# Kernel optimization log

Measured on AMD Instinct MI355X. Metric: run time of the kernel, lower is better.

The kernel has to match this reference:

```python
import jax, jax.numpy as jnp
import numpy as np
import math

# ----- sizes -----
NUM_EDGES = 16384
NUM_NODES = 1024          # senders index into [0, NUM_NODES)
N_MUL = 64                # multiplicity n = V.shape[1]
AVG_NEIGH = 16.0          # avg_num_neighbors
F_IN = 64                 # scalar feature dim of x

# ----- real spherical harmonics (component normalization: sum_m Y_lm^2 = 2l+1) -----
_S3 = math.sqrt(3.0); _S5 = math.sqrt(5.0); _S15 = math.sqrt(15.0)
_C33 = math.sqrt(70.0)/4.0; _C32 = math.sqrt(105.0)/2.0
_C31 = math.sqrt(42.0)/4.0; _C30 = math.sqrt(7.0)/2.0; _CXYZ = math.sqrt(105.0)

def _sph(vn):
    x, y, z = vn[:, 0], vn[:, 1], vn[:, 2]
    Y0 = jnp.ones_like(x)[:, None]
    Y1 = _S3 * vn
    Y2 = jnp.stack([_S15*x*y, _S15*y*z, 0.5*_S5*(3*z*z - 1), _S15*x*z, 0.5*_S15*(x*x - y*y)], axis=1)
    Y3 = jnp.stack([_C33*y*(3*x*x - y*y), _CXYZ*x*y*z, _C31*y*(5*z*z - 1), _C30*z*(5*z*z - 3), _C31*x*(5*z*z - 1), _C32*z*(x*x - y*y), _C33*x*(x*x - 3*y*y)], axis=1)
    return [Y0, Y1, Y2, Y3]

# monomial form of the same SH, used to derive EXACT Clebsch-Gordan coefficients
_SHP = {
    0: [[(1.0, (0,0,0))]],
    1: [[(_S3, (1,0,0))], [(_S3, (0,1,0))], [(_S3, (0,0,1))]],
    2: [[(_S15, (1,1,0))], [(_S15, (0,1,1))], [(1.5*_S5, (0,0,2)), (-0.5*_S5, (0,0,0))], [(_S15, (1,0,1))], [(0.5*_S15, (2,0,0)), (-0.5*_S15, (0,2,0))]],
    3: [[(3*_C33, (2,1,0)), (-_C33, (0,3,0))], [(_CXYZ, (1,1,1))], [(5*_C31, (0,1,2)), (-_C31, (0,1,0))], [(5*_C30, (0,0,3)), (-3*_C30, (0,0,1))], [(5*_C31, (1,0,2)), (-_C31, (1,0,0))], [(_C32, (2,0,1)), (-_C32, (0,2,1))], [(_C33, (3,0,0)), (-3*_C33, (1,2,0))]],
}

def _dfact(n):
    r = 1
    while n > 1:
        r *= n; n -= 2
    return r

def _mono_int(e):
    # exact integral of x^a y^b z^c over the unit sphere
    a, b, c = e
    if (a % 2) or (b % 2) or (c % 2):
        return 0.0
    return 4.0*math.pi*_dfact(a-1)*_dfact(b-1)*_dfact(c-1)/_dfact(a+b+c+1)

def _pmul(p, q):
    return [(cp*cq, (a1+a2, b1+b2, c1+c2)) for cp, (a1,b1,c1) in p for cq, (a2,b2,c2) in q]

def _pint(p):
    return sum(c*_mono_int(e) for c, e in p)

def _cg(l1, l2, l3):
    # unique SO(3) intertwiner in this real-SH basis, scaled like e3nn component norm: sqrt(2l3+1)*w3j
    C = np.zeros((2*l1+1, 2*l2+1, 2*l3+1))
    for i, p1 in enumerate(_SHP[l1]):
        for j, p2 in enumerate(_SHP[l2]):
            p12 = _pmul(p1, p2)
            for k, p3 in enumerate(_SHP[l3]):
                C[i, j, k] = _pint(_pmul(p12, p3)) / (4.0*math.pi)
    return jnp.asarray(C / np.linalg.norm(C) * np.sqrt(2*l3+1), dtype=jnp.float32)

# tensor-product paths surviving filter_ir_out = 0e + 1o + 2e (inputs: SH 0e+1o+2e+3o, V 0e+1o+2e)
_PATHS0 = [(0,0), (1,1), (2,2)]
_PATHS1 = [(0,1), (1,0), (1,2), (2,1), (3,2)]
_PATHS2 = [(0,2), (1,1), (2,0), (2,2), (3,1)]
CGS = {(l1, l2, l3): _cg(l1, l2, l3) for l3, ps in ((0, _PATHS0), (1, _PATHS1), (2, _PATHS2)) for l1, l2 in ps}

# e3nn normalize_function(silu): divide by sqrt(E_{z~N(0,1)}[silu(z)^2])
_zg = np.linspace(-12.0, 12.0, 200001)
_phi = np.exp(-0.5*_zg*_zg)/np.sqrt(2.0*np.pi)
_sl = _zg/(1.0 + np.exp(-_zg))
ACT_C = float(np.sqrt(np.sum(_sl*_sl*_phi)*(_zg[1]-_zg[0])))

def _nsilu(v):
    return jax.nn.silu(v) / ACT_C

def _forward(vectors, x, V, senders, W_w, W1, W2, W3, Wv1, Wv2):
    E, n = V.shape[0], V.shape[1]
    d = jnp.linalg.norm(vectors, axis=1, keepdims=True)                 # [E,1] edge lengths
    vn = vectors / d
    Y = jnp.concatenate(_sph(vn), axis=1)                               # [E,16], ell = 0..3
    w = (x @ W_w) / math.sqrt(x.shape[1])                               # [E,n] edge weights (1-layer MLP, no act)
    wY = w[:, :, None] * Y[:, None, :]                                  # [E,n,16]
    agg = jax.ops.segment_sum(wY, senders, num_segments=NUM_NODES)[senders]  # scatter_sum + map_back
    agg = agg / math.sqrt(AVG_NEIGH)
    A = jnp.split(agg, [1, 4, 9], axis=2)                               # SH chunks: dims 1,3,5,7
    B = jnp.split(V, [1, 4], axis=2)                                    # V chunks: dims 1,3,5
    def tp(l1, l2, l3):
        return jnp.einsum('eni,enj,ijk->enk', A[l1], B[l2], CGS[(l1, l2, l3)])
    scal = jnp.concatenate([tp(a, b, 0) for a, b in _PATHS0], axis=2)   # [E,n,3] new scalars
    V1 = jnp.concatenate([tp(a, b, 1) for a, b in _PATHS1], axis=1)     # [E,5n,3] 1o paths
    V2 = jnp.concatenate([tp(a, b, 2) for a, b in _PATHS2], axis=1)     # [E,5n,5] 2e paths
    h = jnp.concatenate([x, scal.reshape(E, 3*n)], axis=1)              # [E, F_IN+3n]
    h = _nsilu(h @ W1 / math.sqrt(h.shape[1]))
    h = _nsilu(h @ W2 / math.sqrt(W2.shape[0]))
    h = h @ W3 / math.sqrt(W3.shape[0])                                 # output_activation=False
    # poly_envelope(p-1=5, 2), p=6: 1 - 28 d^6 + 48 d^7 - 21 d^8 on [0,1), 0 outside
    u = 1.0 - 28.0*d**6 + 48.0*d**7 - 21.0*d**8
    x_out = jnp.where(d < 1.0, u, 0.0) * h                              # [E,64]
    o1 = jnp.einsum('emi,mo->eoi', V1, Wv1) / math.sqrt(V1.shape[1])    # Linear per irrep: [E,n,3]
    o2 = jnp.einsum('emi,mo->eoi', V2, Wv2) / math.sqrt(V2.shape[1])    # [E,n,5]
    # output 0e block has no input path -> zeros (e3nn Linear, no bias)
    V_out = jnp.concatenate([jnp.zeros((E, n, 1), x_out.dtype), o1, o2], axis=2)  # [E,n,9]
    return x_out, V_out

def setup_inputs():
    key = jax.random.key(0)
    ks = jax.random.split(key, 10)
    E = NUM_EDGES
    vectors = 0.35 * jax.random.normal(ks[0], (E, 3), jnp.float32)   # mostly inside cutoff radius 1
    x = jax.random.normal(ks[1], (E, F_IN), jnp.float32)
    V = jax.random.normal(ks[2], (E, N_MUL, 9), jnp.float32)
    senders = jax.random.randint(ks[3], (E,), 0, NUM_NODES, dtype=jnp.int32)
    W_w = jax.random.normal(ks[4], (F_IN, N_MUL), jnp.float32)
    W1 = jax.random.normal(ks[5], (F_IN + 3*N_MUL, 64), jnp.float32)
    W2 = jax.random.normal(ks[6], (64, 64), jnp.float32)
    W3 = jax.random.normal(ks[7], (64, 64), jnp.float32)
    Wv1 = jax.random.normal(ks[8], (5*N_MUL, N_MUL), jnp.float32)
    Wv2 = jax.random.normal(ks[9], (5*N_MUL, N_MUL), jnp.float32)
    return {"vectors": vectors, "x": x, "V": V, "senders": senders, "W_w": W_w, "W1": W1, "W2": W2, "W3": W3, "Wv1": Wv1, "Wv2": Wv2}

def reference(vectors, x, V, senders, W_w, W1, W2, W3, Wv1, Wv2):
    return _forward(vectors, x, V, senders, W_w, W1, W2, W3, Wv1, Wv2)
```

## Files before the change

### kernel.cpp

```cpp
#include <hip/hip_runtime.h>
#include <math.h>

#define NNODES 1024
#define EB 4

typedef __attribute__((ext_vector_type(8))) short short8;
typedef __attribute__((ext_vector_type(4))) float f32x4;

__device__ __forceinline__ unsigned short f2bf(float f) {
  union { float f; unsigned int u; } v; v.f = f;
  unsigned int r = v.u + 0x7fffu + ((v.u >> 16) & 1u);
  return (unsigned short)(r >> 16);
}

struct CGPack { float v[576]; };

static const double H_SHC[16][2] = {
  {1.0, 0.0},
  {1.7320508075688772, 0.0},
  {1.7320508075688772, 0.0},
  {1.7320508075688772, 0.0},
  {3.8729833462074170, 0.0},
  {3.8729833462074170, 0.0},
  {3.3541019662496844, -1.1180339887498949},
  {3.8729833462074170, 0.0},
  {1.9364916731037085, -1.9364916731037085},
  {6.2749501990055667, -2.0916500663351889},
  {10.246950765959598, 0.0},
  {8.1009258730098255, -1.6201851746019651},
  {6.6143782776614768, -3.9686269665968861},
  {8.1009258730098255, -1.6201851746019651},
  {5.1234753829797990, -5.1234753829797990},
  {2.0916500663351889, -6.2749501990055667},
};
static const int H_SHE[16][2] = {
  {0,0},{1,0},{16,0},{256,0},
  {17,0},{272,0},{512,0},{257,0},{2,32},
  {18,48},{273,0},{528,16},{768,256},{513,1},{258,288},{3,33}};
static const int H_PL1[13] = {0,1,2, 0,1,1,2,3, 0,1,2,2,3};
static const int H_PL2[13] = {0,1,2, 1,0,2,1,2, 2,1,0,2,1};
static const int H_PL3[13] = {0,0,0, 1,1,1,1,1, 2,2,2,2,2};
static const int H_PCG[13] = {0,1,10, 35,44,53,98,143, 248,273,318,343,468};

static double h_dfact(int n) { double r = 1.0; while (n > 1) { r *= n; n -= 2; } return r; }

struct HostConsts {
  CGPack pack;
  float inv_actc;
  HostConsts() {
    const int LOFF[4] = {0,1,4,9};
    for (int p = 0; p < 13; p++) {
      int l1 = H_PL1[p], l2 = H_PL2[p], l3 = H_PL3[p];
      int n1 = 2*l1+1, n2 = 2*l2+1, n3 = 2*l3+1, nent = n1*n2*n3;
      double vals[125], ss = 0.0;
      for (int t = 0; t < nent; t++) {
        int i = t / (n2*n3);
        int rem = t - i*(n2*n3);
        int j = rem / n3;
        int k = rem - j*n3;
        int lm1 = LOFF[l1]+i, lm2 = LOFF[l2]+j, lm3 = LOFF[l3]+k;
        double v = 0.0;
        for (int t1 = 0; t1 < 2; t1++)
        for (int t2 = 0; t2 < 2; t2++)
        for (int t3 = 0; t3 < 2; t3++) {
          double cc = H_SHC[lm1][t1]*H_SHC[lm2][t2]*H_SHC[lm3][t3];
          if (cc == 0.0) continue;
          int s = H_SHE[lm1][t1] + H_SHE[lm2][t2] + H_SHE[lm3][t3];
          int a = s & 15, b = (s >> 4) & 15, c = (s >> 8) & 15;
          if (!((a|b|c) & 1))
            v += cc * (h_dfact(a-1)*h_dfact(b-1)*h_dfact(c-1) / h_dfact(a+b+c+1));
        }
        vals[t] = v; ss += v*v;
      }
      double scale = sqrt((double)(2*l3+1)) / sqrt(ss);
      for (int t = 0; t < nent; t++) pack.v[H_PCG[p]+t] = (float)(vals[t]*scale*0.25);
    }
    pack.v[573] = pack.v[574] = pack.v[575] = 0.f;
    double s = 0.0, dz = 24.0/200000.0;
    for (int i = 0; i <= 200000; i++) {
      double z = -12.0 + dz*i;
      double ph = exp(-0.5*z*z) * 0.39894228040143267794;
      double sl = z / (1.0 + exp(-z));
      s += sl*sl*ph;
    }
    inv_actc = (float)(1.0 / sqrt(s*dz));
  }
};

__global__ __launch_bounds__(256) void k_pre(
    const int* __restrict__ senders, int* __restrict__ counts, int* __restrict__ elist,
    const float* __restrict__ x, const float* __restrict__ Ww,
    float* __restrict__ w_ws,
    const float* __restrict__ Wv1, const float* __restrict__ Wv2,
    const float* __restrict__ W1, const float* __restrict__ W2, const float* __restrict__ W3,
    unsigned short* __restrict__ wv1f, unsigned short* __restrict__ wv2f,
    unsigned short* __restrict__ w1f, unsigned short* __restrict__ w2f,
    unsigned short* __restrict__ w3f,
    float inv_actc, int E)
{
  const int t = threadIdx.x;
  const int bid = blockIdx.x;
  const int nsc = (E + 255) >> 8;

  if (bid < nsc) {
    int e = bid*256 + t;
    if (e < E) {
      int s = senders[e];
      int pos = atomicAdd(&counts[s], 1) & 63;
      elist[s*64 + pos] = e;
    }
    return;
  }

  if (bid < nsc + 32) {
    const int wid = t >> 6, lane = t & 63;
    const int g = (bid - nsc)*4 + wid;
    const float ia = inv_actc;
    const float s320 = 0.05590169943749474f;
    const float* src; unsigned short* dst; int nk, f; float sc;
    if (g < 40)       { src = Wv1; dst = wv1f; nk = 10; f = g;       sc = s320; }
    else if (g < 80)  { src = Wv2; dst = wv2f; nk = 10; f = g - 40;  sc = s320; }
    else if (g < 112) { src = W1;  dst = w1f;  nk = 8;  f = g - 80;  sc = 0.0625f; }
    else if (g < 120) { src = W2;  dst = w2f;  nk = 2;  f = g - 112; sc = 0.125f*ia; }
    else              { src = W3;  dst = w3f;  nk = 2;  f = g - 120; sc = 0.125f*ia; }
    int nt = f / nk;
    int ks = f - nt*nk;
    unsigned short us[8];
    #pragma unroll
    for (int j = 0; j < 8; j++) {
      float v = src[(ks*32 + (lane>>4)*8 + j)*64 + nt*16 + (lane & 15)];
      us[j] = f2bf(v * sc);
    }
    uint4 pk;
    pk.x = (unsigned)us[0] | ((unsigned)us[1] << 16);
    pk.y = (unsigned)us[2] | ((unsigned)us[3] << 16);
    pk.z = (unsigned)us[4] | ((unsigned)us[5] << 16);
    pk.w = (unsigned)us[6] | ((unsigned)us[7] << 16);
    *(uint4*)(dst + ((size_t)f*64 + lane)*8) = pk;
    return;
  }

  __shared__ float xsh[64*64];
  const int eb0 = (bid - nsc - 32) * 64;
  for (int q = t; q < 1024; q += 256)
    ((f32x4*)xsh)[q] = ((const f32x4*)(x + (size_t)eb0*64))[q];

  const int n = t & 63;
  float ww[64];
  #pragma unroll
  for (int f = 0; f < 64; f++) ww[f] = Ww[f*64 + n];
  __syncthreads();

  const int er0 = (t >> 6) * 16;
  #pragma unroll
  for (int i = 0; i < 16; i++) {
    int e = er0 + i;
    const f32x4* xr = (const f32x4*)(&xsh[e*64]);
    float a0 = 0.f, a1 = 0.f, a2 = 0.f, a3 = 0.f;
    #pragma unroll
    for (int fq = 0; fq < 16; fq += 4) {
      f32x4 x0 = xr[fq+0], x1 = xr[fq+1], x2 = xr[fq+2], x3 = xr[fq+3];
      a0 = fmaf(x0.x, ww[fq*4+0],  fmaf(x0.y, ww[fq*4+1],  fmaf(x0.z, ww[fq*4+2],  fmaf(x0.w, ww[fq*4+3],  a0))));
      a1 = fmaf(x1.x, ww[fq*4+4],  fmaf(x1.y, ww[fq*4+5],  fmaf(x1.z, ww[fq*4+6],  fmaf(x1.w, ww[fq*4+7],  a1))));
      a2 = fmaf(x2.x, ww[fq*4+8],  fmaf(x2.y, ww[fq*4+9],  fmaf(x2.z, ww[fq*4+10], fmaf(x2.w, ww[fq*4+11], a2))));
      a3 = fmaf(x3.x, ww[fq*4+12], fmaf(x3.y, ww[fq*4+13], fmaf(x3.z, ww[fq*4+14], fmaf(x3.w, ww[fq*4+15], a3))));
    }
    w_ws[(size_t)(eb0+e)*64 + n] = ((a0+a1)+(a2+a3)) * 0.125f;
  }
}

__global__ __launch_bounds__(256) void k_node(
    const float* __restrict__ vec, const float* __restrict__ w_ws,
    const int* __restrict__ counts, const int* __restrict__ elist,
    float* __restrict__ node_agg)
{
  __shared__ float red[4*1024];
  const int wid = threadIdx.x >> 6, lane = threadIdx.x & 63;
  const int s = blockIdx.x;
  const int deg = min(counts[s], 64);

  const float S3 = 1.7320508075688772f, S5 = 2.23606797749979f, S15 = 3.872983346207417f;
  const float C33 = 2.091650066335189f, C32 = 5.123475382979799f, C31 = 1.6201851746019651f;
  const float C30 = 1.3228756555322954f, CX = 10.246950765959598f;

  float A[16];
  #pragma unroll
  for (int k = 0; k < 16; k++) A[k] = 0.f;

  for (int ii = wid; ii < deg; ii += 4) {
    int e = elist[s*64 + ii];
    float wv = w_ws[(size_t)e*64 + lane];
    float vx = vec[e*3+0], vy = vec[e*3+1], vz = vec[e*3+2];
    float d = sqrtf(vx*vx + vy*vy + vz*vz);
    float X = vx/d, Yv = vy/d, Z = vz/d;
    float y[16];
    y[0] = 1.f;
    y[1] = S3*X;  y[2] = S3*Yv;  y[3] = S3*Z;
    y[4] = S15*X*Yv; y[5] = S15*Yv*Z; y[6] = 0.5f*S5*(3.f*Z*Z - 1.f);
    y[7] = S15*X*Z;  y[8] = 0.5f*S15*(X*X - Yv*Yv);
    y[9]  = C33*Yv*(3.f*X*X - Yv*Yv);
    y[10] = CX*X*Yv*Z;
    y[11] = C31*Yv*(5.f*Z*Z - 1.f);
    y[12] = C30*Z*(5.f*Z*Z - 3.f);
    y[13] = C31*X*(5.f*Z*Z - 1.f);
    y[14] = C32*Z*(X*X - 3.f*Yv*Yv)*0.f + C32*Z*(X*X - Yv*Yv);
    y[14] = C32*Z*(X*X - Yv*Yv);
    y[15] = C33*X*(X*X - 3.f*Yv*Yv);
    #pragma unroll
    for (int k = 0; k < 16; k++) A[k] = fmaf(wv, y[k], A[k]);
  }
  #pragma unroll
  for (int k = 0; k < 16; k++) red[wid*1024 + lane*16 + k] = A[k];
  __syncthreads();
  const int t = threadIdx.x;
  f32x4 v0 = ((f32x4*)red)[t];
  f32x4 v1 = ((f32x4*)red)[256 + t];
  f32x4 v2 = ((f32x4*)red)[512 + t];
  f32x4 v3 = ((f32x4*)red)[768 + t];
  f32x4 sum = v0 + v1 + v2 + v3;
  ((f32x4*)(node_agg + (size_t)s*1024))[t] = sum;
}

template<int L1, int L2, int L3>
__device__ __forceinline__ void tp_path(const float* __restrict__ cgp,
    const float a[16], const float b[9], float o[2*L3+1])
{
  constexpr int N1 = 2*L1+1, N2 = 2*L2+1, N3 = 2*L3+1;
  constexpr int AO = (L1==0) ? 0 : (L1==1) ? 1 : (L1==2) ? 4 : 9;
  constexpr int BO = (L2==0) ? 0 : (L2==1) ? 1 : 4;
  constexpr int LM1 = (L1==0) ? 0 : (L1==1) ? 1 : (L1==2) ? 4 : 9;
  constexpr int LM2 = (L2==0) ? 0 : (L2==1) ? 1 : 4;
  constexpr int LM3 = (L3==0) ? 0 : (L3==1) ? 1 : 4;
  static constexpr unsigned char PAR[16] =
      {0, 1,2,4, 3,6,0,5,0, 2,7,2,4,1,4,1};
  #pragma unroll
  for (int k = 0; k < N3; k++) o[k] = 0.f;
  int ci = 0;
  #pragma unroll
  for (int i = 0; i < N1; i++) {
    #pragma unroll
    for (int j = 0; j < N2; j++) {
      float ab = a[AO+i] * b[BO+j];
      #pragma unroll
      for (int k = 0; k < N3; k++) {
        if ((PAR[LM1+i] ^ PAR[LM2+j] ^ PAR[LM3+k]) == 0)
          o[k] = fmaf(ab, cgp[ci], o[k]);
        ci++;
      }
    }
  }
}

__global__ __launch_bounds__(256, 6) void edge_main(
    const float* __restrict__ vec, const float* __restrict__ x,
    const float* __restrict__ V, const int* __restrict__ senders,
    const float* __restrict__ node_agg, const CGPack P,
    const unsigned short* __restrict__ wv1f, const unsigned short* __restrict__ wv2f,
    const unsigned short* __restrict__ w1f, const unsigned short* __restrict__ w2f,
    const unsigned short* __restrict__ w3f,
    float* __restrict__ out, int E)
{
  __shared__ __align__(16) unsigned short V12sh[32*328];
  __shared__ __align__(16) unsigned short zrow[336];
  __shared__ __align__(16) unsigned short hsh[4*264];
  __shared__ __align__(16) unsigned short h1sh[4*72];
  __shared__ __align__(16) unsigned short h2sh[4*72];
  __shared__ __align__(16) float xosh[4*64];
  __shared__ float ush[EB];

  unsigned short* V1sh = V12sh;
  unsigned short* V2sh = V12sh + 12*328;
  float* vosh = (float*)V12sh;

  const float* cg = P.v;

  const int t = threadIdx.x;
  const int wid = t >> 6, lane = t & 63;
  const int e0 = blockIdx.x * EB;
  const size_t E64 = (size_t)E * 64;

  if (t < 168) ((unsigned int*)zrow)[t] = 0u;

  if (t < 64) {
    int el = t >> 4, off = (t & 15)*4;
    f32x4 xv = *(const f32x4*)(x + (size_t)(e0 + el)*64 + off);
    uint2 pk;
    pk.x = (unsigned)f2bf(xv.x) | ((unsigned)f2bf(xv.y) << 16);
    pk.y = (unsigned)f2bf(xv.z) | ((unsigned)f2bf(xv.w) << 16);
    *(uint2*)(hsh + el*264 + off) = pk;
  }

  {
    const int eloc = wid;
    const int eg = e0 + eloc;

    float b[9];
    const float* vp = V + (size_t)eg*576 + lane*9;
    #pragma unroll
    for (int j = 0; j < 9; j++) b[j] = vp[j];

    const int s = senders[eg];
    float a[16];
    const f32x4* nap = (const f32x4*)(node_agg + s*1024 + lane*16);
    #pragma unroll
    for (int q = 0; q < 4; q++) {
      f32x4 av = nap[q];
      a[q*4+0] = av.x; a[q*4+1] = av.y; a[q*4+2] = av.z; a[q*4+3] = av.w;
    }

    float o1[1], o3[3], o5[5];
    tp_path<0,0,0>(cg + 0,  a, b, o1); hsh[eloc*264 + 64 + lane*3 + 0] = f2bf(o1[0]);
    tp_path<1,1,0>(cg + 1,  a, b, o1); hsh[eloc*264 + 64 + lane*3 + 1] = f2bf(o1[0]);
    tp_path<2,2,0>(cg + 10, a, b, o1); hsh[eloc*264 + 64 + lane*3 + 2] = f2bf(o1[0]);
    tp_path<0,1,1>(cg + 35, a, b, o3);
    { int r = eloc*3; for (int i=0;i<3;i++) V1sh[(r+i)*328 + 0*64 + lane] = f2bf(o3[i]); }
    tp_path<1,0,1>(cg + 44, a, b, o3);
    { int r = eloc*3; for (int i=0;i<3;i++) V1sh[(r+i)*328 + 1*64 + lane] = f2bf(o3[i]); }
    tp_path<1,2,1>(cg + 53, a, b, o3);
    { int r = eloc*3; for (int i=0;i<3;i++) V1sh[(r+i)*328 + 2*64 + lane] = f2bf(o3[i]); }
    tp_path<2,1,1>(cg + 98, a, b, o3);
    { int r = eloc*3; for (int i=0;i<3;i++) V1sh[(r+i)*328 + 3*64 + lane] = f2bf(o3[i]); }
    tp_path<3,2,1>(cg + 143, a, b, o3);
    { int r = eloc*3; for (int i=0;i<3;i++) V1sh[(r+i)*328 + 4*64 + lane] = f2bf(o3[i]); }
    tp_path<0,2,2>(cg + 248, a, b, o5);
    { int r = eloc*5; for (int i=0;i<5;i++) V2sh[(r+i)*328 + 0*64 + lane] = f2bf(o5[i]); }
    tp_path<1,1,2>(cg + 273, a, b, o5);
    { int r = eloc*5; for (int i=0;i<5;i++) V2sh[(r+i)*328 + 1*64 + lane] = f2bf(o5[i]); }
    tp_path<2,0,2>(cg + 318, a, b, o5);
    { int r = eloc*5; for (int i=0;i<5;i++) V2sh[(r+i)*328 + 2*64 + lane] = f2bf(o5[i]); }
    tp_path<2,2,2>(cg + 343, a, b, o5);
    { int r = eloc*5; for (int i=0;i<5;i++) V2sh[(r+i)*328 + 3*64 + lane] = f2bf(o5[i]); }
    tp_path<3,1,2>(cg + 468, a, b, o5);
    { int r = eloc*5; for (int i=0;i<5;i++) V2sh[(r+i)*328 + 4*64 + lane] = f2bf(o5[i]); }

    if (lane == 0) {
      float vx = vec[eg*3+0], vy = vec[eg*3+1], vz = vec[eg*3+2];
      float d = sqrtf(vx*vx + vy*vy + vz*vz);
      float u = 0.f;
      if (d < 1.f) {
        float d3 = d*d*d, d6 = d3*d3, d7 = d6*d, d8 = d7*d;
        u = 1.f - 28.f*d6 + 48.f*d7 - 21.f*d8;
      }
      ush[eloc] = u;
    }
  }
  __syncthreads();

  const int ntile = wid;
  const int qr = lane >> 4;
  const int ml = lane & 15;

  f32x4 acc1 = (f32x4){0,0,0,0};
  {
    const unsigned short* p0 = (ml < 12) ? &V1sh[ml*328] : zrow;
    const unsigned short* bb = wv1f + ((size_t)(ntile*10)*64 + lane)*8;
    #pragma unroll
    for (int ks = 0; ks < 10; ks++) {
      short8 bf = *(const short8*)(bb + ks*512);
      short8 af = *(const short8*)(p0 + ks*32 + qr*8);
      acc1 = __builtin_amdgcn_mfma_f32_16x16x32_bf16(af, bf, acc1, 0, 0, 0);
    }
  }

  f32x4 acc2a = (f32x4){0,0,0,0}, acc2b = (f32x4){0,0,0,0};
  {
    const unsigned short* p0 = &V2sh[ml*328];
    const unsigned short* p1 = (16+ml < 20) ? &V2sh[(16+ml)*328] : zrow;
    const unsigned short* bb = wv2f + ((size_t)(ntile*10)*64 + lane)*8;
    #pragma unroll
    for (int ks = 0; ks < 10; ks++) {
      short8 bf = *(const short8*)(bb + ks*512);
      int ao = ks*32 + qr*8;
      short8 af0 = *(const short8*)(p0 + ao);
      short8 af1 = *(const short8*)(p1 + ao);
      acc2a = __builtin_amdgcn_mfma_f32_16x16x32_bf16(af0, bf, acc2a, 0, 0, 0);
      acc2b = __builtin_amdgcn_mfma_f32_16x16x32_bf16(af1, bf, acc2b, 0, 0, 0);
    }
  }

  const unsigned short* hp = (ml < 4) ? &hsh[ml*264] : zrow;
  {
    f32x4 c = (f32x4){0,0,0,0};
    const unsigned short* bb = w1f + ((size_t)(ntile*8)*64 + lane)*8;
    #pragma unroll
    for (int ks = 0; ks < 8; ks++) {
      short8 bf = *(const short8*)(bb + ks*512);
      short8 af = *(const short8*)(hp + ks*32 + qr*8);
      c = __builtin_amdgcn_mfma_f32_16x16x32_bf16(af, bf, c, 0, 0, 0);
    }
    #pragma unroll
    for (int r = 0; r < 4; r++) {
      int row = qr*4 + r;
      if (row < 4) {
        float v = c[r];
        float sv = v / (1.f + expf(-v));
        h1sh[row*72 + ntile*16 + ml] = f2bf(sv);
      }
    }
  }
  __syncthreads();

  #pragma unroll
  for (int r = 0; r < 4; r++) {
    int row = qr*4 + r;
    if (row < 12) {
      int el = row / 3, i = row - (row/3)*3;
      vosh[el*584 + (ntile*16+ml)*9 + 1 + i] = acc1[r];
    }
  }
  #pragma unroll
  for (int r = 0; r < 4; r++) {
    int row = qr*4 + r;
    int el = row / 5, i = row - (row/5)*5;
    vosh[el*584 + (ntile*16+ml)*9 + 4 + i] = acc2a[r];
  }
  #pragma unroll
  for (int r = 0; r < 4; r++) {
    int row = 16 + qr*4 + r;
    if (row < 20) {
      int el = row / 5, i = row - (row/5)*5;
      vosh[el*584 + (ntile*16+ml)*9 + 4 + i] = acc2b[r];
    }
  }
  { int el = t >> 6, o = t & 63;
    vosh[el*584 + o*9] = 0.f; }

  {
    f32x4 c = (f32x4){0,0,0,0};
    const unsigned short* ap = (ml < 4) ? &h1sh[ml*72] : zrow;
    const unsigned short* bb = w2f + ((size_t)(ntile*2)*64 + lane)*8;
    #pragma unroll
    for (int ks = 0; ks < 2; ks++) {
      short8 bf = *(const short8*)(bb + ks*512);
      short8 af = *(const short8*)(ap + ks*32 + qr*8);
      c = __builtin_amdgcn_mfma_f32_16x16x32_bf16(af, bf, c, 0, 0, 0);
    }
    #pragma unroll
    for (int r = 0; r < 4; r++) {
      int row = qr*4 + r;
      if (row < 4) {
        float v = c[r];
        float sv = v / (1.f + expf(-v));
        h2sh[row*72 + ntile*16 + ml] = f2bf(sv);
      }
    }
  }
  __syncthreads();

  {
    f32x4 c = (f32x4){0,0,0,0};
    const unsigned short* ap = (ml < 4) ? &h2sh[ml*72] : zrow;
    const unsigned short* bb = w3f + ((size_t)(ntile*2)*64 + lane)*8;
    #pragma unroll
    for (int ks = 0; ks < 2; ks++) {
      short8 bf = *(const short8*)(bb + ks*512);
      short8 af = *(const short8*)(ap + ks*32 + qr*8);
      c = __builtin_amdgcn_mfma_f32_16x16x32_bf16(af, bf, c, 0, 0, 0);
    }
    #pragma unroll
    for (int r = 0; r < 4; r++) {
      int row = qr*4 + r;
      if (row < 4) xosh[row*64 + ntile*16 + ml] = ush[row] * c[r];
    }
  }

  for (int q = t; q < 576; q += 256) {
    int el = q / 144, i4 = q - (q/144)*144;
    ((f32x4*)(out + E64 + (size_t)(e0+el)*576))[i4] = ((f32x4*)(vosh + el*584))[i4];
  }
  __syncthreads();

  if (t < 64)
    ((f32x4*)(out + (size_t)e0*64))[t] = ((f32x4*)xosh)[t];
}

extern "C" void kernel_launch(void* const* d_in, const int* in_sizes, int n_in,
                              void* d_out, int out_size, void* d_ws, size_t ws_size,
                              hipStream_t stream)
{
  const float* vec     = (const float*)d_in[0];
  const float* x       = (const float*)d_in[1];
  const float* V       = (const float*)d_in[2];
  const int*   senders = (const int*)  d_in[3];
  const float* Ww      = (const float*)d_in[4];
  const float* W1      = (const float*)d_in[5];
  const float* W2      = (const float*)d_in[6];
  const float* W3      = (const float*)d_in[7];
  const float* Wv1     = (const float*)d_in[8];
  const float* Wv2     = (const float*)d_in[9];
  float* out = (float*)d_out;
  const int E = in_sizes[0] / 3;

  static HostConsts HC;

  char* base = (char*)d_ws;
  float* node_agg = (float*)(base);
  float* w_ws     = (float*)(base + (4<<20));
  int* counts     = (int*)  (base + (8<<20) + 8192);
  int* elist      = (int*)  (base + (8<<20) + 12288);
  unsigned short* wv1f = (unsigned short*)(base + (8<<20) + 278528);
  unsigned short* wv2f = (unsigned short*)(base + (8<<20) + 319488);
  unsigned short* w1f  = (unsigned short*)(base + (8<<20) + 360448);
  unsigned short* w2f  = (unsigned short*)(base + (8<<20) + 393216);
  unsigned short* w3f  = (unsigned short*)(base + (8<<20) + 401408);

  hipMemsetAsync(counts, 0, NNODES*sizeof(int), stream);

  const int nsc = (E + 255) >> 8;
  const int ngemm = (E + 63) >> 6;
  k_pre<<<nsc + 32 + ngemm, 256, 0, stream>>>(senders, counts, elist,
                                      x, Ww, w_ws,
                                      Wv1, Wv2, W1, W2, W3,
                                      wv1f, wv2f, w1f, w2f, w3f, HC.inv_actc, E);
  k_node<<<NNODES, 256, 0, stream>>>(vec, w_ws, counts, elist, node_agg);
  edge_main<<<E/EB, 256, 0, stream>>>(vec, x, V, senders, node_agg, HC.pack,
                                      wv1f, wv2f, w1f, w2f, w3f, out, E);
}
```

Baseline: 165.9 us.

## Stage V tile through LDS, move CG coefficients to global buffer, store x_out directly

Edge kernel now loads the block's V rows with coalesced f32x4 copies into shared memory before per-lane reads, replacing strided 9-float per-lane global loads. CG coefficients are copied once by an extra k_pre block into a workspace buffer and read as a global pointer instead of a 2.3KB kernel-argument struct. The x_out staging buffer and final barrier are removed, writing results straight to global. Adds two extra __syncthreads and shared V overlay that must not clash with V1sh/V2sh writes.

```diff
diff --git a/kernel.cpp b/kernel.cpp
--- a/kernel.cpp
+++ b/kernel.cpp
@@ -96,6 +96,7 @@
     unsigned short* __restrict__ wv1f, unsigned short* __restrict__ wv2f,
     unsigned short* __restrict__ w1f, unsigned short* __restrict__ w2f,
     unsigned short* __restrict__ w3f,
+    const CGPack P, float* __restrict__ cgbuf,
     float inv_actc, int E)
 {
   const int t = threadIdx.x;
@@ -140,8 +141,13 @@
     return;
   }
 
+  if (bid == nsc + 32) {
+    for (int i = t; i < 576; i += 256) cgbuf[i] = P.v[i];
+    return;
+  }
+
   __shared__ float xsh[64*64];
-  const int eb0 = (bid - nsc - 32) * 64;
+  const int eb0 = (bid - nsc - 33) * 64;
   for (int q = t; q < 1024; q += 256)
     ((f32x4*)xsh)[q] = ((const f32x4*)(x + (size_t)eb0*64))[q];
 
@@ -203,7 +209,6 @@
     y[11] = C31*Yv*(5.f*Z*Z - 1.f);
     y[12] = C30*Z*(5.f*Z*Z - 3.f);
     y[13] = C31*X*(5.f*Z*Z - 1.f);
-    y[14] = C32*Z*(X*X - 3.f*Yv*Yv)*0.f + C32*Z*(X*X - Yv*Yv);
     y[14] = C32*Z*(X*X - Yv*Yv);
     y[15] = C33*X*(X*X - 3.f*Yv*Yv);
     #pragma unroll
@@ -254,7 +259,7 @@
 __global__ __launch_bounds__(256, 6) void edge_main(
     const float* __restrict__ vec, const float* __restrict__ x,
     const float* __restrict__ V, const int* __restrict__ senders,
-    const float* __restrict__ node_agg, const CGPack P,
+    const float* __restrict__ node_agg, const float* __restrict__ cg,
     const unsigned short* __restrict__ wv1f, const unsigned short* __restrict__ wv2f,
     const unsigned short* __restrict__ w1f, const unsigned short* __restrict__ w2f,
     const unsigned short* __restrict__ w3f,
@@ -265,14 +270,12 @@
   __shared__ __align__(16) unsigned short hsh[4*264];
   __shared__ __align__(16) unsigned short h1sh[4*72];
   __shared__ __align__(16) unsigned short h2sh[4*72];
-  __shared__ __align__(16) float xosh[4*64];
   __shared__ float ush[EB];
 
   unsigned short* V1sh = V12sh;
   unsigned short* V2sh = V12sh + 12*328;
   float* vosh = (float*)V12sh;
-
-  const float* cg = P.v;
+  float* vsta = ((float*)V12sh) + 2944;
 
   const int t = threadIdx.x;
   const int wid = t >> 6, lane = t & 63;
@@ -291,22 +294,27 @@
   }
 
   {
+    const f32x4* vsrc = (const f32x4*)(V + (size_t)e0*576);
+    f32x4* vdst = (f32x4*)vsta;
+    for (int q = t; q < 576; q += 256) vdst[q] = vsrc[q];
+  }
+  __syncthreads();
+
+  {
     const int eloc = wid;
     const int eg = e0 + eloc;
 
     float b[9];
-    const float* vp = V + (size_t)eg*576 + lane*9;
-    #pragma unroll
-    for (int j = 0; j < 9; j++) b[j] = vp[j];
+    #pragma unroll
+    for (int j = 0; j < 9; j++) b[j] = vsta[eloc*576 + lane*9 + j];
 
     const int s = senders[eg];
     float a[16];
-    const f32x4* nap = (const f32x4*)(node_agg + s*1024 + lane*16);
-    #pragma unroll
-    for (int q = 0; q < 4; q++) {
-      f32x4 av = nap[q];
-      a[q*4+0] = av.x; a[q*4+1] = av.y; a[q*4+2] = av.z; a[q*4+3] = av.w;
-    }
+    const float* nap = node_agg + s*1024 + lane*16;
+    #pragma unroll
+    for (int k = 0; k < 16; k++) a[k] = nap[k];
+
+    __syncthreads();
 
     float o1[1], o3[3], o5[5];
     tp_path<0,0,0>(cg + 0,  a, b, o1); hsh[eloc*264 + 64 + lane*3 + 0] = f2bf(o1[0]);
@@ -460,7 +468,9 @@
     #pragma unroll
     for (int r = 0; r < 4; r++) {
       int row = qr*4 + r;
-      if (row < 4) xosh[row*64 + ntile*16 + ml] = ush[row] * c[r];
+      if (row < 4) {
+        out[(size_t)(e0+row)*64 + ntile*16 + ml] = ush[row] * c[r];
+      }
     }
   }
 
@@ -468,10 +478,6 @@
     int el = q / 144, i4 = q - (q/144)*144;
     ((f32x4*)(out + E64 + (size_t)(e0+el)*576))[i4] = ((f32x4*)(vosh + el*584))[i4];
   }
-  __syncthreads();
-
-  if (t < 64)
-    ((f32x4*)(out + (size_t)e0*64))[t] = ((f32x4*)xosh)[t];
 }
 
 extern "C" void kernel_launch(void* const* d_in, const int* in_sizes, int n_in,
@@ -496,8 +502,9 @@
   char* base = (char*)d_ws;
   float* node_agg = (float*)(base);
   float* w_ws     = (float*)(base + (4<<20));
+  float* cgbuf    = (float*)(base + (8<<20));
   int* counts     = (int*)  (base + (8<<20) + 8192);
-  int* elist      = (int*)  (base + (8<<20) + 12288);
+  int* elist      = (int*)  (base + (8<<20) + 16384);
   unsigned short* wv1f = (unsigned short*)(base + (8<<20) + 278528);
   unsigned short* wv2f = (unsigned short*)(base + (8<<20) + 319488);
   unsigned short* w1f  = (unsigned short*)(base + (8<<20) + 360448);
@@ -508,11 +515,12 @@
 
   const int nsc = (E + 255) >> 8;
   const int ngemm = (E + 63) >> 6;
-  k_pre<<<nsc + 32 + ngemm, 256, 0, stream>>>(senders, counts, elist,
+  k_pre<<<nsc + 33 + ngemm, 256, 0, stream>>>(senders, counts, elist,
                                       x, Ww, w_ws,
                                       Wv1, Wv2, W1, W2, W3,
-                                      wv1f, wv2f, w1f, w2f, w3f, HC.inv_actc, E);
+                                      wv1f, wv2f, w1f, w2f, w3f,
+                                      HC.pack, cgbuf, HC.inv_actc, E);
   k_node<<<NNODES, 256, 0, stream>>>(vec, w_ws, counts, elist, node_agg);
-  edge_main<<<E/EB, 256, 0, stream>>>(vec, x, V, senders, node_agg, HC.pack,
+  edge_main<<<E/EB, 256, 0, stream>>>(vec, x, V, senders, node_agg, cgbuf,
                                       wv1f, wv2f, w1f, w2f, w3f, out, E);
 }
```

Result: faster. 158.9 us (-4.2%).
